# Performance work log

Hardware: AMD Instinct MI355X
Metric: run time of the kernel (lower is better)

The kernel has to match this reference:

```python
import jax, jax.numpy as jnp
import numpy as np

LEN = 20_000_000  # samples per channel (interleaved real/imag), divisible by 10


def setup_inputs() -> dict:
    key = jax.random.key(0)
    k0, k1, k2, k3 = jax.random.split(key, 4)
    in0 = jax.random.normal(k0, (LEN,), dtype=jnp.float32)
    in1 = jax.random.normal(k1, (LEN,), dtype=jnp.float32)
    in2 = jax.random.normal(k2, (LEN,), dtype=jnp.float32)
    in3 = jax.random.normal(k3, (LEN,), dtype=jnp.float32)
    # bf buffer: ones with imaginary parts (odd indices) zeroed
    bf = jnp.ones((1, 8), dtype=jnp.float32).at[0, 1::2].set(0.0)
    return {"in0": in0, "in1": in1, "in2": in2, "in3": in3, "bf": bf}


def reference(in0, in1, in2, in3, bf):
    # Deinterleave real/imag, stack channels -> (4, N), reshape to (B, 4, 5)
    in_real = jnp.stack((in0[::2], in1[::2], in2[::2], in3[::2]), axis=0).reshape(-1, 4, 5)
    in_imag = jnp.stack((in0[1::2], in1[1::2], in2[1::2], in3[1::2]), axis=0).reshape(-1, 4, 5)
    bf_real = bf[0, ::2].reshape(1, 1, 4)
    bf_imag = bf[0, 1::2].reshape(1, 1, 4)
    # Complex matmul: (1,1,4) @ (B,4,5) -> (B,1,5)
    out_real = jnp.matmul(bf_real, in_real) - jnp.matmul(bf_imag, in_imag)
    out_imag = jnp.matmul(bf_imag, in_real) + jnp.matmul(bf_real, in_imag)
    result = jnp.concatenate([out_real, out_imag], axis=2)  # (B,1,10)
    # Faithful to original: strided scatter on dim 1 (size 1) -> no-op copy
    result2 = jnp.zeros_like(result)
    result2 = result2.at[:, ::2].set(result[:, :5])
    result2 = result2.at[:, 1::2].set(result[:, 5:])
    return result2
```

## Files before the change

kernel.cpp:

```cpp
#include <hip/hip_runtime.h>
#include <hip/hip_bf16.h>


__global__ __launch_bounds__(256) void beamform_kernel(
    const float* __restrict__ in0, const float* __restrict__ in1,
    const float* __restrict__ in2, const float* __restrict__ in3,
    const float* __restrict__ bf, float* __restrict__ out,
    int blocksPerChannel)
{
    const int bl = blockIdx.x * blockDim.x + threadIdx.x;
    if (bl >= blocksPerChannel) return;
    const int ch = blockIdx.y;

    const float* in = (ch == 0) ? in0 : (ch == 1) ? in1 : (ch == 2) ? in2 : in3;

    const float4* p = reinterpret_cast<const float4*>(in + (size_t)bl * 40);
    float x[40];
#pragma unroll
    for (int k = 0; k < 10; ++k) {
        float4 v = p[k];
        x[4 * k + 0] = v.x;
        x[4 * k + 1] = v.y;
        x[4 * k + 2] = v.z;
        x[4 * k + 3] = v.w;
    }

    float br[4], bi[4];
#pragma unroll
    for (int r = 0; r < 4; ++r) {
        br[r] = bf[2 * r];
        bi[r] = bf[2 * r + 1];
    }

    float o[10];
#pragma unroll
    for (int c = 0; c < 5; ++c) {
        float re = 0.f, im = 0.f;
#pragma unroll
        for (int r = 0; r < 4; ++r) {
            const float xr = x[10 * r + 2 * c];
            const float xi = x[10 * r + 2 * c + 1];
            re += br[r] * xr - bi[r] * xi;
            im += bi[r] * xr + br[r] * xi;
        }
        o[c] = re;
        o[5 + c] = im;
    }

    const size_t b = (size_t)ch * blocksPerChannel + bl;
    float2* q = reinterpret_cast<float2*>(out + b * 10);
#pragma unroll
    for (int k = 0; k < 5; ++k) {
        q[k] = make_float2(o[2 * k], o[2 * k + 1]);
    }
}

extern "C" void kernel_launch(void* const* d_in, const int* in_sizes, int n_in,
                              void* d_out, int out_size, void* d_ws, size_t ws_size,
                              hipStream_t stream)
{
    const float* in0 = (const float*)d_in[0];
    const float* in1 = (const float*)d_in[1];
    const float* in2 = (const float*)d_in[2];
    const float* in3 = (const float*)d_in[3];
    const float* bf  = (const float*)d_in[4];
    float* out = (float*)d_out;

    const int len = in_sizes[0];
    const int blocksPerChannel = len / 40;

    const int block = 256;
    dim3 grid((blocksPerChannel + block - 1) / block, 4, 1);
    beamform_kernel<<<grid, dim3(block, 1, 1), 0, stream>>>(
        in0, in1, in2, in3, bf, out, blocksPerChannel);
}
```

Before: 300.0 us.

## Split each 40-sample block across five threads for coalesced float2 loads

Instead of one thread loading 40 floats via ten float4 loads and computing five complex outputs, each block is now handled by five threads. Each computes one output column from four float2 loads and writes two scalar outputs. This makes neighbouring lanes read adjacent memory instead of addresses 160 bytes apart, improving coalescing and cutting per-thread register use. The cost is five times more threads, an integer divide, and narrower scalar stores.

```diff
diff --git a/kernel.cpp b/kernel.cpp
--- a/kernel.cpp
+++ b/kernel.cpp
@@ -6,53 +6,43 @@
     const float* __restrict__ in0, const float* __restrict__ in1,
     const float* __restrict__ in2, const float* __restrict__ in3,
     const float* __restrict__ bf, float* __restrict__ out,
-    int blocksPerChannel)
+    int blocksPerChannel, int threadsPerChannel)
 {
-    const int bl = blockIdx.x * blockDim.x + threadIdx.x;
-    if (bl >= blocksPerChannel) return;
+    const int tid = blockIdx.x * blockDim.x + threadIdx.x;
+    if (tid >= threadsPerChannel) return;
     const int ch = blockIdx.y;
 
-    const float* in = (ch == 0) ? in0 : (ch == 1) ? in1 : (ch == 2) ? in2 : in3;
+    const float* __restrict__ in =
+        (ch == 0) ? in0 : (ch == 1) ? in1 : (ch == 2) ? in2 : in3;
 
-    const float4* p = reinterpret_cast<const float4*>(in + (size_t)bl * 40);
-    float x[40];
-#pragma unroll
-    for (int k = 0; k < 10; ++k) {
-        float4 v = p[k];
-        x[4 * k + 0] = v.x;
-        x[4 * k + 1] = v.y;
-        x[4 * k + 2] = v.z;
-        x[4 * k + 3] = v.w;
-    }
+    const int bl = tid / 5;
+    const int c  = tid - bl * 5;
 
-    float br[4], bi[4];
-#pragma unroll
-    for (int r = 0; r < 4; ++r) {
-        br[r] = bf[2 * r];
-        bi[r] = bf[2 * r + 1];
-    }
+    const float2* __restrict__ p =
+        reinterpret_cast<const float2*>(in + (size_t)bl * 40 + 2 * c);
+    const float2 x0 = p[0];
+    const float2 x1 = p[5];
+    const float2 x2 = p[10];
+    const float2 x3 = p[15];
 
-    float o[10];
-#pragma unroll
-    for (int c = 0; c < 5; ++c) {
-        float re = 0.f, im = 0.f;
-#pragma unroll
-        for (int r = 0; r < 4; ++r) {
-            const float xr = x[10 * r + 2 * c];
-            const float xi = x[10 * r + 2 * c + 1];
-            re += br[r] * xr - bi[r] * xi;
-            im += bi[r] * xr + br[r] * xi;
-        }
-        o[c] = re;
-        o[5 + c] = im;
-    }
+    const float br0 = bf[0], bi0 = bf[1];
+    const float br1 = bf[2], bi1 = bf[3];
+    const float br2 = bf[4], bi2 = bf[5];
+    const float br3 = bf[6], bi3 = bf[7];
+
+    float re = br0 * x0.x - bi0 * x0.y;
+    float im = bi0 * x0.x + br0 * x0.y;
+    re += br1 * x1.x - bi1 * x1.y;
+    im += bi1 * x1.x + br1 * x1.y;
+    re += br2 * x2.x - bi2 * x2.y;
+    im += bi2 * x2.x + br2 * x2.y;
+    re += br3 * x3.x - bi3 * x3.y;
+    im += bi3 * x3.x + br3 * x3.y;
 
     const size_t b = (size_t)ch * blocksPerChannel + bl;
-    float2* q = reinterpret_cast<float2*>(out + b * 10);
-#pragma unroll
-    for (int k = 0; k < 5; ++k) {
-        q[k] = make_float2(o[2 * k], o[2 * k + 1]);
-    }
+    float* __restrict__ o = out + b * 10;
+    o[c] = re;
+    o[5 + c] = im;
 }
 
 extern "C" void kernel_launch(void* const* d_in, const int* in_sizes, int n_in,
@@ -68,9 +58,10 @@
 
     const int len = in_sizes[0];
     const int blocksPerChannel = len / 40;
+    const int threadsPerChannel = blocksPerChannel * 5;
 
     const int block = 256;
-    dim3 grid((blocksPerChannel + block - 1) / block, 4, 1);
+    dim3 grid((threadsPerChannel + block - 1) / block, 4, 1);
     beamform_kernel<<<grid, dim3(block, 1, 1), 0, stream>>>(
-        in0, in1, in2, in3, bf, out, blocksPerChannel);
+        in0, in1, in2, in3, bf, out, blocksPerChannel, threadsPerChannel);
 }
```

Result: faster. 287.0 us (-4.3%).
